# Kernel optimization log

Measured on AMD Instinct MI355X. Metric: run time of the kernel, lower is better.

The kernel has to match this reference:

```python
import jax, jax.numpy as jnp
import numpy as np

STEPS, BATCH = 2048, 512
INPUT_DIM = 16          # climate features after stripping flow channel
STORE_DIM = 8           # number of conceptual stores S
HIDDEN = 128
SLOW = 2                # SLOW_STORE index
RAIN_IDX = 0            # rain column within sliced climate inputs
OUT_DIM = STORE_DIM * (STORE_DIM + 2)   # flow_between_stores=True -> 80
IN_DIM_FLOWNET = INPUT_DIM + STORE_DIM  # 24


def setup_inputs() -> dict:
    key = jax.random.key(0)
    ks = jax.random.split(key, 10)
    hyd_input = jax.random.uniform(ks[0], (STEPS, BATCH, 1 + INPUT_DIM), dtype=jnp.float32)
    s = 0.05
    W0 = jax.random.normal(ks[1], (HIDDEN, IN_DIM_FLOWNET), dtype=jnp.float32) * s
    b0 = jax.random.normal(ks[2], (HIDDEN,), dtype=jnp.float32) * s
    W1 = jax.random.normal(ks[3], (HIDDEN, HIDDEN), dtype=jnp.float32) * s
    b1 = jax.random.normal(ks[4], (HIDDEN,), dtype=jnp.float32) * s
    W_in = jax.random.normal(ks[5], (STORE_DIM + 1, HIDDEN), dtype=jnp.float32) * s
    b_in = jax.random.normal(ks[6], (STORE_DIM + 1,), dtype=jnp.float32) * s
    W_out = jax.random.normal(ks[7], (OUT_DIM, HIDDEN), dtype=jnp.float32) * s
    b_out = jax.random.normal(ks[8], (OUT_DIM,), dtype=jnp.float32) * s - 3.0  # bias.data -= 3
    return {"hyd_input": hyd_input, "W0": W0, "b0": b0, "W1": W1, "b1": b1,
            "W_in": W_in, "b_in": b_in, "W_out": W_out, "b_out": b_out}


def reference(hyd_input, W0, b0, W1, b1, W_in, b_in, W_out, b_out):
    S = STORE_DIM
    flow = hyd_input[:, :, 0]          # [T, B] observed flow
    x = hyd_input[:, :, 1:]            # [T, B, F] climate forcings
    rain = x[:, :, RAIN_IDX]           # [T, B]
    # correct_init_baseflow: 25th percentile of observed flow over time, per batch elem
    baseflow = jnp.percentile(flow, 25.0, axis=0)  # [B]

    B = x.shape[1]
    stores0 = jnp.zeros((B, S), dtype=hyd_input.dtype).at[:, 1].set(1.0)  # init_stores

    def step(stores, inp):
        x_t, rain_t, is_first = inp
        # flownet: (num_layers=2) Linear -> ReLU (dropout is eval-mode identity)
        h = jnp.concatenate([x_t, 0.01 * stores], axis=1)      # [B, F+S]
        h = jax.nn.relu(h @ W0.T + b0)
        h = jax.nn.relu(h @ W1.T + b1)
        # inflow gating (softmax over S+1): distribute rain into stores
        a = jax.nn.softmax(h @ W_in.T + b_in, axis=-1)          # [B, S+1]
        stores = stores + a[:, 1:] * rain_t[:, None]
        # outflow fluxes (sigmoid), S*(S+2) = inter-store | escape | flow
        b = jax.nn.sigmoid(h @ W_out.T + b_out)                 # [B, S*(S+2)]
        # sequential inter-store transfers (order matters; S is small/fixed)
        for d in range(S):
            fb = b[:, d * S:(d + 1) * S] * stores               # [B, S]
            stores = (stores - fb).at[:, d].add(fb.sum(axis=1))
        escape = b[:, -2 * S:-S] * stores
        stores = stores - escape
        b_flow = b[:, -S:]
        flow_distn = b_flow * stores
        stores = stores - flow_distn
        # at i==0: overwrite slow store from baseflow / outflow coeff
        corrected = stores.at[:, SLOW].set(baseflow / jnp.maximum(b_flow[:, SLOW], 1e-5))
        stores = jnp.where(is_first, corrected, stores)
        return stores, flow_distn.sum(axis=1)

    is_first = jnp.arange(x.shape[0]) == 0
    _, flows = jax.lax.scan(step, stores0, (x, rain, is_first))
    return flows  # [T, B]
```

## Files before the change

kernel.cpp:

```cpp
#include <hip/hip_runtime.h>
#include <hip/hip_bf16.h>
#include <math.h>

#define STEPS 2048
#define BATCH 512

typedef __attribute__((ext_vector_type(8))) short short8;
typedef __attribute__((ext_vector_type(4))) short short4v;
typedef __attribute__((ext_vector_type(2))) short short2v;
typedef __attribute__((ext_vector_type(4))) float f32x4;
typedef __attribute__((ext_vector_type(2))) float f32x2;

__device__ __forceinline__ short f2bf(float f) {
    union { float f; unsigned u; } v; v.f = f;
    unsigned u = v.u;
    return (short)((u + 0x7FFFu + ((u >> 16) & 1u)) >> 16);
}
__device__ __forceinline__ short2v pk2(float a, float b) {
    __hip_bfloat162 h = __float22bfloat162_rn(make_float2(a, b));
    union { __hip_bfloat162 h; short2v s; } u; u.h = h; return u.s;
}

#define LBAR() do { asm volatile("s_waitcnt lgkmcnt(0)" ::: "memory"); \
                    __builtin_amdgcn_s_barrier();                      \
                    asm volatile("" ::: "memory"); } while (0)

__global__ __launch_bounds__(256) void baseflow_kernel(
    const float* __restrict__ hyd, float* __restrict__ bf)
{
    __shared__ float arr[STEPS];
    const int b = blockIdx.x;
    const int tid = threadIdx.x;
    for (int t = tid; t < STEPS; t += 256)
        arr[t] = hyd[(size_t)(t * BATCH + b) * 17];
    __syncthreads();
    for (int k = 2; k <= STEPS; k <<= 1) {
        for (int j = k >> 1; j > 0; j >>= 1) {
            for (int i = tid; i < STEPS; i += 256) {
                int ixj = i ^ j;
                if (ixj > i) {
                    float a = arr[i], c = arr[ixj];
                    bool up = ((i & k) == 0);
                    if (up ? (a > c) : (a < c)) { arr[i] = c; arr[ixj] = a; }
                }
            }
            __syncthreads();
        }
    }
    if (tid == 0) bf[b] = arr[511] + 0.75f * (arr[512] - arr[511]);
}

__global__ __launch_bounds__(256, 1) void hyd_step_kernel(
    const float* __restrict__ hyd,
    const float* __restrict__ W0,  const float* __restrict__ b0,
    const float* __restrict__ W1,  const float* __restrict__ b1,
    const float* __restrict__ Win, const float* __restrict__ bin,
    const float* __restrict__ Wout,const float* __restrict__ bout,
    const float* __restrict__ baseflow,
    float* __restrict__ out)
{
    __shared__ __align__(16) short h1F[256 * 8];
    __shared__ __align__(16) short h2F[256 * 8];
    __shared__ __align__(16) float hb[2][100];

    const int tid  = threadIdx.x;
    const int blk  = blockIdx.x;
    const int lane = tid & 63;
    const int wv   = tid >> 6;
    const int cn   = lane & 15;
    const int cg   = lane >> 4;
    const int col  = lane & 1;

    for (int i = tid; i < 256 * 8; i += 256) { h1F[i] = 0; h2F[i] = 0; }

    short8 a0[2]; f32x4 c0[2];
    short8 a1[2][4]; f32x4 c1[2];
    short8 ah[2][4]; f32x4 ch[2];
    #pragma unroll
    for (int i = 0; i < 2; ++i) {
        const int mt = 2 * wv + i;
        const int row = mt * 16 + cn;
        #pragma unroll
        for (int j = 0; j < 8; ++j) {
            int k = cg * 8 + j;
            float w = 0.f;
            if (k < 16)      w = W0[row * 24 + k];
            else if (k < 24) w = 0.01f * W0[row * 24 + k];
            a0[i][j] = f2bf(w);
        }
        #pragma unroll
        for (int kt = 0; kt < 4; ++kt)
            #pragma unroll
            for (int j = 0; j < 8; ++j)
                a1[i][kt][j] = f2bf(W1[row * 128 + kt * 32 + cg * 8 + j]);
        #pragma unroll
        for (int r = 0; r < 4; ++r) {
            int m = mt * 16 + cg * 4 + r;
            c0[i][r] = b0[m];
            c1[i][r] = b1[m];
        }
    }
    const int nht = (wv == 1 || wv == 2) ? 2 : 1;
    int htile[2];
    htile[0] = (wv == 0) ? 0 : (wv == 1) ? 1 : (wv == 2) ? 3 : 5;
    htile[1] = htile[0] + ((nht == 2) ? 1 : 0);
    #pragma unroll
    for (int i = 0; i < 2; ++i) {
        const int ht = htile[i];
        const int row = ht * 16 + cn;
        #pragma unroll
        for (int kt = 0; kt < 4; ++kt)
            #pragma unroll
            for (int j = 0; j < 8; ++j) {
                int k = kt * 32 + cg * 8 + j;
                float w = 0.f;
                if (row != 1) {
                    int q = (row == 0) ? 0 : (row - 1);
                    if (q < 9)       w = Win[q * 128 + k];
                    else if (q < 89) w = Wout[(q - 9) * 128 + k];
                }
                ah[i][kt][j] = f2bf(w);
            }
        #pragma unroll
        for (int r = 0; r < 4; ++r) {
            int m = ht * 16 + cg * 4 + r;
            float bb = 0.f;
            if (m != 1) {
                int q = (m == 0) ? 0 : (m - 1);
                if (q < 9)       bb = bin[q];
                else if (q < 89) bb = bout[q - 9];
            }
            ch[i][r] = bb;
        }
    }

    f32x2 s01 = {0.f, 1.f}, s23 = {0.f, 0.f}, s45 = {0.f, 0.f}, s67 = {0.f, 0.f};
    const float bfv = baseflow[blk * 2 + col];
    short8 spack;
    {
        short2v p0 = pk2(s01.x, s01.y);
        short2v p1 = pk2(s23.x, s23.y);
        short2v p2 = pk2(s45.x, s45.y);
        short2v p3 = pk2(s67.x, s67.y);
        spack[0] = p0[0]; spack[1] = p0[1]; spack[2] = p1[0]; spack[3] = p1[1];
        spack[4] = p2[0]; spack[5] = p2[1]; spack[6] = p3[0]; spack[7] = p3[1];
    }

    const bool xlane = (cn < 2) && (cg < 2);
    const int xoff = (blk * 2 + cn) * 17 + 1 + cg * 8;
    const int roff = (blk * 2 + col) * 17 + 1;
    float xv[8];
    float rain_next;
    if (xlane) {
        const float* p = hyd + xoff;
        #pragma unroll
        for (int j = 0; j < 8; ++j) xv[j] = p[j];
    }
    rain_next = hyd[roff];

    f32x4 accx0, accx1;
    {
        short8 xfrag = 0;
        if (xlane) {
            short2v q0 = pk2(xv[0], xv[1]), q1 = pk2(xv[2], xv[3]),
                    q2 = pk2(xv[4], xv[5]), q3 = pk2(xv[6], xv[7]);
            xfrag[0] = q0[0]; xfrag[1] = q0[1]; xfrag[2] = q1[0]; xfrag[3] = q1[1];
            xfrag[4] = q2[0]; xfrag[5] = q2[1]; xfrag[6] = q3[0]; xfrag[7] = q3[1];
        }
        accx0 = __builtin_amdgcn_mfma_f32_16x16x32_bf16(a0[0], xfrag, c0[0], 0, 0, 0);
        accx1 = __builtin_amdgcn_mfma_f32_16x16x32_bf16(a0[1], xfrag, c0[1], 0, 0, 0);
    }

    for (int t = 0; t < STEPS; ++t) {
        const float rain = rain_next;
        const int tn = (t + 1 < STEPS) ? (t + 1) : t;
        const float* px = hyd + (size_t)tn * (BATCH * 17);
        if (xlane) {
            const float* p = px + xoff;
            #pragma unroll
            for (int j = 0; j < 8; ++j) xv[j] = p[j];
        }
        rain_next = px[roff];

        short8 sfrag = 0;
        if (cn < 2 && cg == 2) sfrag = spack;
        #pragma unroll
        for (int i = 0; i < 2; ++i) {
            f32x4 acc = __builtin_amdgcn_mfma_f32_16x16x32_bf16(
                a0[i], sfrag, (i ? accx1 : accx0), 0, 0, 0);
            if (cn < 2) {
                int m0 = (2 * wv + i) * 16 + cg * 4;
                short4v p;
                short2v pa = pk2(fmaxf(acc[0], 0.f), fmaxf(acc[1], 0.f));
                short2v pb = pk2(fmaxf(acc[2], 0.f), fmaxf(acc[3], 0.f));
                p[0] = pa[0]; p[1] = pa[1]; p[2] = pb[0]; p[3] = pb[1];
                *(short4v*)&h1F[((m0 >> 3) * 16 + cn) * 8 + (m0 & 7)] = p;
            }
        }
        LBAR();

        short8 bf1[4];
        #pragma unroll
        for (int kt = 0; kt < 4; ++kt)
            bf1[kt] = *(const short8*)&h1F[(kt * 64 + lane) * 8];
        #pragma unroll
        for (int i = 0; i < 2; ++i) {
            f32x4 zz = {0.f, 0.f, 0.f, 0.f};
            f32x4 accA = __builtin_amdgcn_mfma_f32_16x16x32_bf16(a1[i][0], bf1[0], c1[i], 0, 0, 0);
            accA = __builtin_amdgcn_mfma_f32_16x16x32_bf16(a1[i][1], bf1[1], accA, 0, 0, 0);
            f32x4 accB = __builtin_amdgcn_mfma_f32_16x16x32_bf16(a1[i][2], bf1[2], zz, 0, 0, 0);
            accB = __builtin_amdgcn_mfma_f32_16x16x32_bf16(a1[i][3], bf1[3], accB, 0, 0, 0);
            f32x4 acc = accA + accB;
            if (cn < 2) {
                int m0 = (2 * wv + i) * 16 + cg * 4;
                short4v p;
                short2v pa = pk2(fmaxf(acc[0], 0.f), fmaxf(acc[1], 0.f));
                short2v pb = pk2(fmaxf(acc[2], 0.f), fmaxf(acc[3], 0.f));
                p[0] = pa[0]; p[1] = pa[1]; p[2] = pb[0]; p[3] = pb[1];
                *(short4v*)&h2F[((m0 >> 3) * 16 + cn) * 8 + (m0 & 7)] = p;
            }
        }
        LBAR();

        short8 bf2[4];
        #pragma unroll
        for (int kt = 0; kt < 4; ++kt)
            bf2[kt] = *(const short8*)&h2F[(kt * 64 + lane) * 8];
        #pragma unroll
        for (int i = 0; i < 2; ++i) {
            if (i < nht) {
                f32x4 zz = {0.f, 0.f, 0.f, 0.f};
                f32x4 accA = __builtin_amdgcn_mfma_f32_16x16x32_bf16(ah[i][0], bf2[0], ch[i], 0, 0, 0);
                accA = __builtin_amdgcn_mfma_f32_16x16x32_bf16(ah[i][1], bf2[1], accA, 0, 0, 0);
                f32x4 accB = __builtin_amdgcn_mfma_f32_16x16x32_bf16(ah[i][2], bf2[2], zz, 0, 0, 0);
                accB = __builtin_amdgcn_mfma_f32_16x16x32_bf16(ah[i][3], bf2[3], accB, 0, 0, 0);
                f32x4 acc = accA + accB;
                if (cn < 2) {
                    const int ht = htile[i];
                    f32x4 o;
                    if (ht == 0) {
                        #pragma unroll
                        for (int r = 0; r < 4; ++r) {
                            int m = cg * 4 + r;
                            float v = acc[r];
                            bool isl = (m < 10);
                            float em = __expf(isl ? v : -v);
                            o[r] = isl ? em : __builtin_amdgcn_rcpf(1.f + em);
                        }
                    } else {
                        #pragma unroll
                        for (int r = 0; r < 4; ++r) {
                            float em = __expf(-acc[r]);
                            o[r] = __builtin_amdgcn_rcpf(1.f + em);
                        }
                    }
                    *(f32x4*)&hb[cn][ht * 16 + cg * 4] = o;
                }
            }
        }
        LBAR();

        f32x4 gqA[11];
        #pragma unroll
        for (int c2 = 0; c2 < 11; ++c2)
            gqA[c2] = *(const f32x4*)&hb[col][c2 * 4];
        {
            short8 xfrag = 0;
            if (xlane) {
                short2v q0 = pk2(xv[0], xv[1]), q1 = pk2(xv[2], xv[3]),
                        q2 = pk2(xv[4], xv[5]), q3 = pk2(xv[6], xv[7]);
                xfrag[0] = q0[0]; xfrag[1] = q0[1]; xfrag[2] = q1[0]; xfrag[3] = q1[1];
                xfrag[4] = q2[0]; xfrag[5] = q2[1]; xfrag[6] = q3[0]; xfrag[7] = q3[1];
            }
            accx0 = __builtin_amdgcn_mfma_f32_16x16x32_bf16(a0[0], xfrag, c0[0], 0, 0, 0);
            accx1 = __builtin_amdgcn_mfma_f32_16x16x32_bf16(a0[1], xfrag, c0[1], 0, 0, 0);
        }

        const float* gvA = (const float*)gqA;
        const f32x2* gA2 = (const f32x2*)gqA;
        {
            f32x2 dt = (gA2[1] + gA2[2]) + (gA2[3] + gA2[4]);
            float den = gvA[0] + dt.x + dt.y;
            float rr = rain * __builtin_amdgcn_rcpf(den);
            f32x2 rr2 = {rr, rr};
            s01 += gA2[1] * rr2; s23 += gA2[2] * rr2;
            s45 += gA2[3] * rr2; s67 += gA2[4] * rr2;

            #pragma unroll
            for (int d = 0; d < 4; ++d) {
                const int gb = 5 + 4 * d;
                f32x2 fb0 = gA2[gb + 0] * s01, fb1 = gA2[gb + 1] * s23;
                f32x2 fb2 = gA2[gb + 2] * s45, fb3 = gA2[gb + 3] * s67;
                f32x2 tt = (fb0 + fb1) + (fb2 + fb3);
                float fs = tt.x + tt.y;
                s01 -= fb0; s23 -= fb1; s45 -= fb2; s67 -= fb3;
                if      (d == 0) s01.x += fs;
                else if (d == 1) s01.y += fs;
                else if (d == 2) s23.x += fs;
                else             s23.y += fs;
            }
        }

        f32x4 gqB[13];
        #pragma unroll
        for (int c2 = 0; c2 < 13; ++c2)
            gqB[c2] = *(const f32x4*)&hb[col][40 + c2 * 4];
        const float* gvB = (const float*)gqB;
        const f32x2* gB2 = (const f32x2*)gqB;
        {
            #pragma unroll
            for (int d = 4; d < 8; ++d) {
                const int gb = 4 * d - 15;
                f32x2 fb0 = gB2[gb + 0] * s01, fb1 = gB2[gb + 1] * s23;
                f32x2 fb2 = gB2[gb + 2] * s45, fb3 = gB2[gb + 3] * s67;
                f32x2 tt = (fb0 + fb1) + (fb2 + fb3);
                float fs = tt.x + tt.y;
                s01 -= fb0; s23 -= fb1; s45 -= fb2; s67 -= fb3;
                if      (d == 4) s45.x += fs;
                else if (d == 5) s45.y += fs;
                else if (d == 6) s67.x += fs;
                else             s67.y += fs;
            }
            s01 -= gB2[17] * s01; s23 -= gB2[18] * s23;
            s45 -= gB2[19] * s45; s67 -= gB2[20] * s67;
            f32x2 f0 = gB2[21] * s01, f1 = gB2[22] * s23;
            f32x2 f2 = gB2[23] * s45, f3 = gB2[24] * s67;
            f32x2 ft = (f0 + f1) + (f2 + f3);
            float fsum = ft.x + ft.y;
            s01 -= f0; s23 -= f1; s45 -= f2; s67 -= f3;
            if (t == 0) s23.x = bfv / fmaxf(gvB[44], 1e-5f);

            {
                short2v p0 = pk2(s01.x, s01.y);
                short2v p1 = pk2(s23.x, s23.y);
                short2v p2 = pk2(s45.x, s45.y);
                short2v p3 = pk2(s67.x, s67.y);
                spack[0] = p0[0]; spack[1] = p0[1]; spack[2] = p1[0]; spack[3] = p1[1];
                spack[4] = p2[0]; spack[5] = p2[1]; spack[6] = p3[0]; spack[7] = p3[1];
            }
            if (tid < 2) out[(size_t)t * BATCH + blk * 2 + tid] = fsum;
        }
    }
}

extern "C" void kernel_launch(void* const* d_in, const int* in_sizes, int n_in,
                              void* d_out, int out_size, void* d_ws, size_t ws_size,
                              hipStream_t stream)
{
    const float* hyd  = (const float*)d_in[0];
    const float* W0   = (const float*)d_in[1];
    const float* b0   = (const float*)d_in[2];
    const float* W1   = (const float*)d_in[3];
    const float* b1   = (const float*)d_in[4];
    const float* Win  = (const float*)d_in[5];
    const float* bin  = (const float*)d_in[6];
    const float* Wout = (const float*)d_in[7];
    const float* bout = (const float*)d_in[8];
    float* out = (float*)d_out;
    float* bf  = (float*)d_ws;

    baseflow_kernel<<<BATCH, 256, 0, stream>>>(hyd, bf);
    hyd_step_kernel<<<BATCH / 2, 256, 0, stream>>>(
        hyd, W0, b0, W1, b1, Win, bin, Wout, bout, bf, out);
}
```

Baseline: 2.917 ms.

## Compute first layer redundantly per wave to drop a block barrier

Each wave now computes all eight first-layer tiles itself and writes them to a private per-wave LDS buffer. The block-wide barrier between layer 0 and layer 1 becomes a wave-local LDS wait, which takes one barrier out of the per-step critical path of the sequential scan. In exchange every wave issues four times as many layer-0 MFMAs, holds more registers for weights and accumulators, and uses more LDS.

```diff
diff --git a/kernel.cpp b/kernel.cpp
--- a/kernel.cpp
+++ b/kernel.cpp
@@ -24,6 +24,7 @@
 #define LBAR() do { asm volatile("s_waitcnt lgkmcnt(0)" ::: "memory"); \
                     __builtin_amdgcn_s_barrier();                      \
                     asm volatile("" ::: "memory"); } while (0)
+#define WFENCE() asm volatile("s_waitcnt lgkmcnt(0)" ::: "memory")
 
 __global__ __launch_bounds__(256) void baseflow_kernel(
     const float* __restrict__ hyd, float* __restrict__ bf)
@@ -59,7 +60,7 @@
     const float* __restrict__ baseflow,
     float* __restrict__ out)
 {
-    __shared__ __align__(16) short h1F[256 * 8];
+    __shared__ __align__(16) short h1W[4][256 * 8];
     __shared__ __align__(16) short h2F[256 * 8];
     __shared__ __align__(16) float hb[2][100];
 
@@ -71,14 +72,14 @@
     const int cg   = lane >> 4;
     const int col  = lane & 1;
 
-    for (int i = tid; i < 256 * 8; i += 256) { h1F[i] = 0; h2F[i] = 0; }
-
-    short8 a0[2]; f32x4 c0[2];
+    for (int i = lane; i < 256 * 8; i += 64) h1W[wv][i] = 0;
+    for (int i = tid; i < 256 * 8; i += 256) h2F[i] = 0;
+
+    short8 a0[8]; f32x4 c0[8];
     short8 a1[2][4]; f32x4 c1[2];
     short8 ah[2][4]; f32x4 ch[2];
     #pragma unroll
-    for (int i = 0; i < 2; ++i) {
-        const int mt = 2 * wv + i;
+    for (int mt = 0; mt < 8; ++mt) {
         const int row = mt * 16 + cn;
         #pragma unroll
         for (int j = 0; j < 8; ++j) {
@@ -86,19 +87,24 @@
             float w = 0.f;
             if (k < 16)      w = W0[row * 24 + k];
             else if (k < 24) w = 0.01f * W0[row * 24 + k];
-            a0[i][j] = f2bf(w);
-        }
+            a0[mt][j] = f2bf(w);
+        }
+        #pragma unroll
+        for (int r = 0; r < 4; ++r)
+            c0[mt][r] = b0[mt * 16 + cg * 4 + r];
+    }
+    #pragma unroll
+    for (int i = 0; i < 2; ++i) {
+        const int mt = 2 * wv + i;
+        const int row = mt * 16 + cn;
         #pragma unroll
         for (int kt = 0; kt < 4; ++kt)
             #pragma unroll
             for (int j = 0; j < 8; ++j)
                 a1[i][kt][j] = f2bf(W1[row * 128 + kt * 32 + cg * 8 + j]);
         #pragma unroll
-        for (int r = 0; r < 4; ++r) {
-            int m = mt * 16 + cg * 4 + r;
-            c0[i][r] = b0[m];
-            c1[i][r] = b1[m];
-        }
+        for (int r = 0; r < 4; ++r)
+            c1[i][r] = b1[mt * 16 + cg * 4 + r];
     }
     const int nht = (wv == 1 || wv == 2) ? 2 : 1;
     int htile[2];
@@ -158,7 +164,7 @@
     }
     rain_next = hyd[roff];
 
-    f32x4 accx0, accx1;
+    f32x4 accx[8];
     {
         short8 xfrag = 0;
         if (xlane) {
@@ -167,9 +173,12 @@
             xfrag[0] = q0[0]; xfrag[1] = q0[1]; xfrag[2] = q1[0]; xfrag[3] = q1[1];
             xfrag[4] = q2[0]; xfrag[5] = q2[1]; xfrag[6] = q3[0]; xfrag[7] = q3[1];
         }
-        accx0 = __builtin_amdgcn_mfma_f32_16x16x32_bf16(a0[0], xfrag, c0[0], 0, 0, 0);
-        accx1 = __builtin_amdgcn_mfma_f32_16x16x32_bf16(a0[1], xfrag, c0[1], 0, 0, 0);
-    }
+        #pragma unroll
+        for (int mt = 0; mt < 8; ++mt)
+            accx[mt] = __builtin_amdgcn_mfma_f32_16x16x32_bf16(a0[mt], xfrag, c0[mt], 0, 0, 0);
+    }
+
+    LBAR();
 
     for (int t = 0; t < STEPS; ++t) {
         const float rain = rain_next;
@@ -185,24 +194,23 @@
         short8 sfrag = 0;
         if (cn < 2 && cg == 2) sfrag = spack;
         #pragma unroll
-        for (int i = 0; i < 2; ++i) {
-            f32x4 acc = __builtin_amdgcn_mfma_f32_16x16x32_bf16(
-                a0[i], sfrag, (i ? accx1 : accx0), 0, 0, 0);
+        for (int mt = 0; mt < 8; ++mt) {
+            f32x4 acc = __builtin_amdgcn_mfma_f32_16x16x32_bf16(a0[mt], sfrag, accx[mt], 0, 0, 0);
             if (cn < 2) {
-                int m0 = (2 * wv + i) * 16 + cg * 4;
+                int m0 = mt * 16 + cg * 4;
                 short4v p;
                 short2v pa = pk2(fmaxf(acc[0], 0.f), fmaxf(acc[1], 0.f));
                 short2v pb = pk2(fmaxf(acc[2], 0.f), fmaxf(acc[3], 0.f));
                 p[0] = pa[0]; p[1] = pa[1]; p[2] = pb[0]; p[3] = pb[1];
-                *(short4v*)&h1F[((m0 >> 3) * 16 + cn) * 8 + (m0 & 7)] = p;
-            }
-        }
-        LBAR();
+                *(short4v*)&h1W[wv][((m0 >> 3) * 16 + cn) * 8 + (m0 & 7)] = p;
+            }
+        }
+        WFENCE();
 
         short8 bf1[4];
         #pragma unroll
         for (int kt = 0; kt < 4; ++kt)
-            bf1[kt] = *(const short8*)&h1F[(kt * 64 + lane) * 8];
+            bf1[kt] = *(const short8*)&h1W[wv][(kt * 64 + lane) * 8];
         #pragma unroll
         for (int i = 0; i < 2; ++i) {
             f32x4 zz = {0.f, 0.f, 0.f, 0.f};
@@ -272,8 +280,9 @@
                 xfrag[0] = q0[0]; xfrag[1] = q0[1]; xfrag[2] = q1[0]; xfrag[3] = q1[1];
                 xfrag[4] = q2[0]; xfrag[5] = q2[1]; xfrag[6] = q3[0]; xfrag[7] = q3[1];
             }
-            accx0 = __builtin_amdgcn_mfma_f32_16x16x32_bf16(a0[0], xfrag, c0[0], 0, 0, 0);
-            accx1 = __builtin_amdgcn_mfma_f32_16x16x32_bf16(a0[1], xfrag, c0[1], 0, 0, 0);
+            #pragma unroll
+            for (int mt = 0; mt < 8; ++mt)
+                accx[mt] = __builtin_amdgcn_mfma_f32_16x16x32_bf16(a0[mt], xfrag, c0[mt], 0, 0, 0);
         }
 
         const float* gvA = (const float*)gqA;
```

Measured after the change: 3.672 ms. 25.9% more time.
